# Optimization experiments

Measured on AMD Instinct MI355X. Metric: run time of the kernel, lower is better.

The kernel has to match this reference:

```python
import jax, jax.numpy as jnp
import numpy as np
import math

HEADS = 8
DIM_HEAD = 64

def setup_inputs() -> dict:
    key = jax.random.key(0)
    ks = jax.random.split(key, 6)
    B, L, D = 2, 2048, 512
    Ls = 1936
    inner = HEADS * DIM_HEAD  # 512
    x = jax.random.normal(ks[0], (B, L, D), dtype=jnp.float32)
    positions = jax.random.normal(ks[1], (B, Ls, 2), dtype=jnp.float32) * 10.0
    w_qkv = jax.random.normal(ks[2], (3 * inner, D), dtype=jnp.float32) * (1.0 / math.sqrt(D))
    w_out = jax.random.normal(ks[3], (D, inner), dtype=jnp.float32) * (1.0 / math.sqrt(inner))
    b_out = jnp.zeros((D,), dtype=jnp.float32)
    log_sigma = jnp.full((HEADS,), math.log(3.0), dtype=jnp.float32)
    global_bias = jnp.float32(0.0)
    return {"x": x, "positions": positions, "w_qkv": w_qkv, "w_out": w_out,
            "b_out": b_out, "log_sigma": log_sigma, "global_bias": global_bias,
            "num_spatial": Ls}

def reference(x, positions, w_qkv, w_out, b_out, log_sigma, global_bias, num_spatial):
    B, L, D = x.shape
    H, Dh = HEADS, DIM_HEAD
    scale = Dh ** (-0.5)
    # qkv projection: [B,L,3*H*Dh] -> q,k,v each [B,H,L,Dh]
    qkv = jnp.einsum('bld,ed->ble', x, w_qkv)
    q, k, v = jnp.split(qkv, 3, axis=-1)
    def heads(t):
        return t.reshape(B, L, H, Dh).transpose(0, 2, 1, 3)
    q, k, v = heads(q), heads(k), heads(v)
    attn = jnp.einsum('bhid,bhjd->bhij', q, k) * scale  # [B,H,L,L]
    # Gaussian distance bias on the spatial block, global_bias elsewhere
    Ls = num_spatial
    diff = positions[:, :, None, :] - positions[:, None, :, :]  # [B,Ls,Ls,2]
    dist_sq = jnp.sum(diff * diff, axis=-1)                     # [B,Ls,Ls]
    sigma_sq = jnp.exp(log_sigma) ** 2                          # [H]
    spatial_bias = -dist_sq[:, None] / (2.0 * sigma_sq[None, :, None, None])  # [B,H,Ls,Ls]
    full_bias = jnp.full((B, H, L, L), global_bias, dtype=x.dtype)
    full_bias = full_bias.at[:, :, :Ls, :Ls].set(spatial_bias)
    attn = jax.nn.softmax(attn + full_bias, axis=-1)
    out = jnp.einsum('bhij,bhjd->bhid', attn, v)  # [B,H,L,Dh]
    out = out.transpose(0, 2, 1, 3).reshape(B, L, H * Dh)
    return jnp.einsum('ble,de->bld', out, w_out) + b_out
```

## Files before the change

### kernel.cpp

```cpp
#include <hip/hip_runtime.h>
#include <stdint.h>
#include <stddef.h>

#define NB   2
#define NL   2048
#define ND   512
#define NH   8
#define DH   64
#define LOG2E 1.44269504f
#define NIT  16
#define RG_TOT 32768
#define JS   4

typedef __attribute__((ext_vector_type(8))) short bf16x8;
typedef __attribute__((ext_vector_type(4))) float f32x4;

__device__ __forceinline__ unsigned short f2bf(float f) {
  union { float f; unsigned int u; } c; c.f = f;
  unsigned int u = c.u;
  unsigned int r = u + 0x7fffu + ((u >> 16) & 1u);
  return (unsigned short)(r >> 16);
}

__device__ __forceinline__ float bf2f(unsigned short u) {
  union { unsigned int i; float f; } c; c.i = ((unsigned int)u) << 16; return c.f;
}

__device__ __forceinline__ float fexp2(float x) {
#if __has_builtin(__builtin_amdgcn_exp2f)
  return __builtin_amdgcn_exp2f(x);
#else
  return exp2f(x);
#endif
}

__device__ __forceinline__ void gl_lds16(const unsigned short* g, unsigned short* l) {
#if __has_builtin(__builtin_amdgcn_global_load_lds)
  __builtin_amdgcn_global_load_lds(
      (const __attribute__((address_space(1))) unsigned int*)g,
      (__attribute__((address_space(3))) unsigned int*)l, 16, 0, 0);
#else
  *(uint4*)l = *(const uint4*)g;
#endif
}

#define XC  524288
#define WQC 196608
#define WOC 65536
#define TOTC (XC + WQC + WOC)
__global__ void cvt_f32_bf16(const float* __restrict__ x, const float* __restrict__ wq,
                             const float* __restrict__ wo, const float* __restrict__ positions,
                             const int* __restrict__ ns_p,
                             unsigned short* __restrict__ xb, unsigned short* __restrict__ wqb,
                             unsigned short* __restrict__ wob, float* __restrict__ pospad) {
  int idx = blockIdx.x * 256 + threadIdx.x;
  if (idx < TOTC) {
    const float* src; unsigned short* dst; int off;
    if (idx < XC)            { src = x;  dst = xb;  off = idx; }
    else if (idx < XC + WQC) { src = wq; dst = wqb; off = idx - XC; }
    else                     { src = wo; dst = wob; off = idx - XC - WQC; }
    float4 f = ((const float4*)src)[off];
    ushort4 o;
    o.x = f2bf(f.x); o.y = f2bf(f.y); o.z = f2bf(f.z); o.w = f2bf(f.w);
    ((ushort4*)dst)[off] = o;
  } else {
    int i2 = idx - TOTC;
    if (i2 < NB * 1024) {
      int b = i2 >> 10;
      int jj = (i2 & 1023) * 2;
      int Ls = ns_p[0];
      float4 o = make_float4(0.f, 0.f, 0.f, 0.f);
      if (jj < Ls) { o.x = positions[((size_t)b * Ls + jj) * 2];
                     o.y = positions[((size_t)b * Ls + jj) * 2 + 1]; }
      if (jj + 1 < Ls) { o.z = positions[((size_t)b * Ls + jj + 1) * 2];
                         o.w = positions[((size_t)b * Ls + jj + 1) * 2 + 1]; }
      *(float4*)&pospad[((size_t)b * NL + jj) * 2] = o;
    }
  }
}

template<int MODE, int MT>
__global__ __launch_bounds__(256, 2) void gemm_bf16(
    const unsigned short* __restrict__ A, const unsigned short* __restrict__ Bm,
    const float* __restrict__ bias,
    unsigned short* __restrict__ qo, unsigned short* __restrict__ kp,
    unsigned short* __restrict__ vo, float* __restrict__ out, int K)
{
  constexpr int MB = MT / 32;
  constexpr int AC = MT * 4;
  constexpr int TC = AC + 512;
  __shared__ __align__(16) unsigned short S[MT * 32 + 128 * 32];
  const int tid = threadIdx.x, wid = tid >> 6, lane = tid & 63;
  const int quad = lane >> 4, l15 = lane & 15;
  const int m0 = blockIdx.x * MT, n0 = blockIdx.y * 128;
  const int wm = (wid >> 1) * (MT / 2), wn = (wid & 1) * 64;

  f32x4 acc[MB][4];
#pragma unroll
  for (int a = 0; a < MB; ++a)
#pragma unroll
    for (int b = 0; b < 4; ++b)
#pragma unroll
      for (int z = 0; z < 4; ++z) acc[a][b][z] = 0.f;

  for (int k0 = 0; k0 < K; k0 += 32) {
#pragma unroll
    for (int p = 0; p < TC / 256; ++p) {
      int c = p * 256 + wid * 64 + lane;
      if (c < AC) {
        int row = c >> 2, off = c & 3;
        gl_lds16(A + (size_t)(m0 + row) * K + k0 + off * 8, &S[c * 8]);
      } else {
        int cb = c - AC;
        int row = cb >> 2, off = cb & 3;
        gl_lds16(Bm + (size_t)(n0 + row) * K + k0 + off * 8, &S[c * 8]);
      }
    }
    __syncthreads();
    bf16x8 af[MB], bfr[4];
#pragma unroll
    for (int mb = 0; mb < MB; ++mb)
      af[mb] = *(const bf16x8*)&S[(wm + mb * 16 + l15) * 32 + quad * 8];
#pragma unroll
    for (int nb = 0; nb < 4; ++nb)
      bfr[nb] = *(const bf16x8*)&S[MT * 32 + (wn + nb * 16 + l15) * 32 + quad * 8];
#pragma unroll
    for (int mb = 0; mb < MB; ++mb)
#pragma unroll
      for (int nb = 0; nb < 4; ++nb)
        acc[mb][nb] = __builtin_amdgcn_mfma_f32_16x16x32_bf16(af[mb], bfr[nb], acc[mb][nb], 0, 0, 0);
    __syncthreads();
  }

  const float QSCALE = 0.125f * LOG2E;
#pragma unroll
  for (int mb = 0; mb < MB; ++mb) {
    int e0 = m0 + wm + mb * 16 + quad * 4;
    if (MODE == 0) {
      int s   = e0 >> 9;
      int hh  = (e0 >> 6) & 7;
      if (s == 1) {
        int kc  = mb >> 1;
        int q_t = ((mb & 1) << 1) + (quad >> 1);
        int par = quad & 1;
#pragma unroll
        for (int nb = 0; nb < 4; ++nb) {
          int token = n0 + wn + nb * 16 + l15;
          int bb = token >> 11, ll = token & 2047;
          int jt = ll >> 4;
          ushort4 o;
          o.x = f2bf(acc[mb][nb][0]);
          o.y = f2bf(acc[mb][nb][1]);
          o.z = f2bf(acc[mb][nb][2]);
          o.w = f2bf(acc[mb][nb][3]);
          size_t addr = (((size_t)(bb * NH + hh) * 128 + jt) * 2 + kc) * 512
                      + (q_t * 16 + l15) * 8 + par * 4;
          *(ushort4*)&kp[addr] = o;
        }
      } else {
        unsigned short* dst = (s == 0) ? qo : vo;
        float sc = (s == 0) ? QSCALE : 1.0f;
        int dh0 = e0 & 63;
#pragma unroll
        for (int nb = 0; nb < 4; ++nb) {
          int token = n0 + wn + nb * 16 + l15;
          int bb = token >> 11, ll = token & 2047;
          ushort4 o;
          o.x = f2bf(acc[mb][nb][0] * sc);
          o.y = f2bf(acc[mb][nb][1] * sc);
          o.z = f2bf(acc[mb][nb][2] * sc);
          o.w = f2bf(acc[mb][nb][3] * sc);
          *(ushort4*)&dst[(((size_t)bb * NH + hh) * NL + ll) * DH + dh0] = o;
        }
      }
    } else {
      float4 bv = *(const float4*)&bias[e0];
#pragma unroll
      for (int nb = 0; nb < 4; ++nb) {
        int token = n0 + wn + nb * 16 + l15;
        float4 o;
        o.x = acc[mb][nb][0] + bv.x;
        o.y = acc[mb][nb][1] + bv.y;
        o.z = acc[mb][nb][2] + bv.z;
        o.w = acc[mb][nb][3] + bv.w;
        *(float4*)&out[(size_t)token * ND + e0] = o;
      }
    }
  }
}

__global__ __launch_bounds__(256) void repack_v(const unsigned short* __restrict__ v,
                                                unsigned short* __restrict__ vp) {
  __shared__ unsigned short T[64][74];
  const int l0 = blockIdx.x * 64;
  const int bh = blockIdx.y;
  const unsigned short* src = v + ((size_t)bh * NL + l0) * DH;
  unsigned short* dst = vp + (size_t)bh * 131072 + (size_t)(l0 >> 5) * 2048;
#pragma unroll
  for (int p = 0; p < 2; ++p) {
    int c = p * 256 + threadIdx.x;
    int row = c >> 3, seg = c & 7;
    *(uint4*)&T[row][seg * 8] = *(const uint4*)(src + row * DH + seg * 8);
  }
  __syncthreads();
#pragma unroll
  for (int p = 0; p < 2; ++p) {
    int c = p * 256 + threadIdx.x;
    int l15 = c & 15, q = (c >> 4) & 3, dht = (c >> 6) & 3, jcl = c >> 8;
    unsigned short u[8];
#pragma unroll
    for (int t = 0; t < 8; ++t) u[t] = T[jcl * 32 + q * 8 + t][dht * 16 + l15];
    *(uint4*)(dst + (size_t)jcl * 2048 + dht * 512 + (q * 16 + l15) * 8) = *(uint4*)u;
  }
}

__global__ __launch_bounds__(256, 2) void flash_kernel(
    const unsigned short* __restrict__ qb, const unsigned short* __restrict__ kp,
    const unsigned short* __restrict__ vp, const float* __restrict__ pospad,
    const float* __restrict__ log_sigma, const float* __restrict__ gbias_p,
    const int* __restrict__ ns_p, unsigned short* __restrict__ Pb, float* __restrict__ rsbuf)
{
  const int it = blockIdx.x >> 2;
  const int js = blockIdx.x & 3;
  const int h  = blockIdx.y;
  const int b  = blockIdx.z;
  const int i0 = it * 128;
  const int jbase = js * (NL / JS);
  const int Ls = ns_p[0];
  const float gb  = gbias_p[0];
  const float sig = __expf(log_sigma[h]);
  const float CI  = LOG2E * 0.5f / (sig * sig);
  const float A2  = 2.0f * CI;
  const float LGB = LOG2E * gb;
  const float CBL = -8.0f * LOG2E + LGB;

  const int tid  = threadIdx.x;
  const int wid  = tid >> 6;
  const int lane = tid & 63;
  const int quad = lane >> 4;
  const int l15  = lane & 15;

  __shared__ __align__(16) unsigned short Ps[128][76];

  const size_t bh = (size_t)b * NH + h;
  const unsigned short* qbase = qb + (bh * NL + i0) * DH;
  const unsigned short* kpb   = kp + bh * 131072;
  const unsigned short* vpb   = vp + bh * 131072;
  const float* posb = pospad + (size_t)b * NL * 2;

  bf16x8 af[2][2];
#pragma unroll
  for (int mb = 0; mb < 2; ++mb)
#pragma unroll
    for (int kc = 0; kc < 2; ++kc)
      af[mb][kc] = *(const bf16x8*)(qbase + (size_t)(wid * 32 + mb * 16 + l15) * DH + kc * 32 + quad * 8);

  float pix_[2][4], piy_[2][4], riCm[2][4], ispf[2][4];
#pragma unroll
  for (int mb = 0; mb < 2; ++mb)
#pragma unroll
    for (int r = 0; r < 4; ++r) {
      int ig = i0 + wid * 32 + mb * 16 + quad * 4 + r;
      float2 p2 = *(const float2*)(posb + (size_t)ig * 2);
      pix_[mb][r] = p2.x; piy_[mb][r] = p2.y;
      ispf[mb][r] = (ig < Ls) ? 1.f : 0.f;
      riCm[mb][r] = -(CI * (p2.x * p2.x + p2.y * p2.y)) - LGB;
    }

  f32x4 accO[2][4];
  float rsum[2][4];
#pragma unroll
  for (int mb = 0; mb < 2; ++mb) {
#pragma unroll
    for (int d = 0; d < 4; ++d)
#pragma unroll
      for (int z = 0; z < 4; ++z) accO[mb][d][z] = 0.f;
#pragma unroll
    for (int r = 0; r < 4; ++r) rsum[mb][r] = 0.f;
  }

  for (int jt = 0; jt < NL / JS / 64; ++jt) {
    const int j0 = jbase + jt * 64;

    bf16x8 kf[4][2];
#pragma unroll
    for (int nb = 0; nb < 4; ++nb)
#pragma unroll
      for (int kc = 0; kc < 2; ++kc)
        kf[nb][kc] = *(const bf16x8*)(kpb + ((size_t)((j0 >> 4) + nb) * 2 + kc) * 512 + lane * 8);

    float pjx2[4], pjy2[4], rjC[4], jspf[4];
#pragma unroll
    for (int nb = 0; nb < 4; ++nb) {
      int jg = j0 + nb * 16 + l15;
      float2 p2 = *(const float2*)(posb + (size_t)jg * 2);
      pjx2[nb] = A2 * p2.x; pjy2[nb] = A2 * p2.y;
      rjC[nb]  = -(CI * (p2.x * p2.x + p2.y * p2.y));
      jspf[nb] = (jg < Ls) ? 1.f : 0.f;
    }

    f32x4 accS[2][4];
#pragma unroll
    for (int mb = 0; mb < 2; ++mb)
#pragma unroll
      for (int nb = 0; nb < 4; ++nb) {
#pragma unroll
        for (int z = 0; z < 4; ++z) accS[mb][nb][z] = 0.f;
        accS[mb][nb] = __builtin_amdgcn_mfma_f32_16x16x32_bf16(af[mb][0], kf[nb][0], accS[mb][nb], 0, 0, 0);
        accS[mb][nb] = __builtin_amdgcn_mfma_f32_16x16x32_bf16(af[mb][1], kf[nb][1], accS[mb][nb], 0, 0, 0);
      }

    bf16x8 vf[4][2];
#pragma unroll
    for (int dht = 0; dht < 4; ++dht)
#pragma unroll
      for (int jc = 0; jc < 2; ++jc)
        vf[dht][jc] = *(const bf16x8*)(vpb + ((size_t)((j0 >> 5) + jc) * 4 + dht) * 512 + lane * 8);

#pragma unroll
    for (int mb = 0; mb < 2; ++mb)
#pragma unroll
      for (int nb = 0; nb < 4; ++nb)
#pragma unroll
        for (int r = 0; r < 4; ++r) {
          float u = riCm[mb][r] + rjC[nb];
          u = __builtin_fmaf(piy_[mb][r], pjy2[nb], u);
          u = __builtin_fmaf(pix_[mb][r], pjx2[nb], u);
          float msp = ispf[mb][r] * jspf[nb];
          float t = __builtin_fmaf(msp, u, accS[mb][nb][r] + CBL);
          float p = fexp2(t);
          rsum[mb][r] += p;
          Ps[wid * 32 + mb * 16 + quad * 4 + r][nb * 16 + l15] = f2bf(p);
        }

    bf16x8 pf[2][2];
#pragma unroll
    for (int mb = 0; mb < 2; ++mb)
#pragma unroll
      for (int jc = 0; jc < 2; ++jc)
        pf[mb][jc] = *(const bf16x8*)&Ps[wid * 32 + mb * 16 + l15][jc * 32 + quad * 8];
#pragma unroll
    for (int mb = 0; mb < 2; ++mb)
#pragma unroll
      for (int dht = 0; dht < 4; ++dht) {
        accO[mb][dht] = __builtin_amdgcn_mfma_f32_16x16x32_bf16(pf[mb][0], vf[dht][0], accO[mb][dht], 0, 0, 0);
        accO[mb][dht] = __builtin_amdgcn_mfma_f32_16x16x32_bf16(pf[mb][1], vf[dht][1], accO[mb][dht], 0, 0, 0);
      }
  }

#pragma unroll
  for (int mb = 0; mb < 2; ++mb)
#pragma unroll
    for (int r = 0; r < 4; ++r) {
      float v = rsum[mb][r];
      v += __shfl_xor(v, 1);
      v += __shfl_xor(v, 2);
      v += __shfl_xor(v, 4);
      v += __shfl_xor(v, 8);
      rsum[mb][r] = v;
    }
  const size_t rgbase = (bh * NIT + it) * 128;
  const size_t poff = (size_t)js * RG_TOT * DH;
#pragma unroll
  for (int mb = 0; mb < 2; ++mb)
#pragma unroll
    for (int r = 0; r < 4; ++r) {
      int row = wid * 32 + mb * 16 + quad * 4 + r;
#pragma unroll
      for (int dht = 0; dht < 4; ++dht)
        Pb[poff + (rgbase + row) * DH + dht * 16 + l15] = f2bf(accO[mb][dht][r]);
      if (l15 == 0)
        rsbuf[(size_t)js * RG_TOT + rgbase + row] = rsum[mb][r];
    }
}

__global__ __launch_bounds__(256) void combine_kernel(const unsigned short* __restrict__ Pb,
                                                      const float* __restrict__ rsbuf,
                                                      unsigned short* __restrict__ attnb) {
  int idx = blockIdx.x * 256 + threadIdx.x;
  int rg = idx >> 4, c4 = idx & 15;
  float s0 = 0.f, s1 = 0.f, s2 = 0.f, s3 = 0.f, rsum = 0.f;
#pragma unroll
  for (int js = 0; js < JS; ++js) {
    ushort4 u = *(const ushort4*)&Pb[((size_t)js * RG_TOT + rg) * DH + c4 * 4];
    s0 += bf2f(u.x); s1 += bf2f(u.y); s2 += bf2f(u.z); s3 += bf2f(u.w);
    rsum += rsbuf[(size_t)js * RG_TOT + rg];
  }
  float rs = 1.0f / rsum;
  int bhm = rg >> 11;
  int l   = rg & 2047;
  int bb  = bhm >> 3, hh = bhm & 7;
  ushort4 o;
  o.x = f2bf(s0 * rs);
  o.y = f2bf(s1 * rs);
  o.z = f2bf(s2 * rs);
  o.w = f2bf(s3 * rs);
  *(ushort4*)&attnb[(((size_t)bb * NL + l) * ND) + hh * DH + c4 * 4] = o;
}

extern "C" void kernel_launch(void* const* d_in, const int* in_sizes, int n_in,
                              void* d_out, int out_size, void* d_ws, size_t ws_size,
                              hipStream_t stream) {
  const float* x         = (const float*)d_in[0];
  const float* positions = (const float*)d_in[1];
  const float* w_qkv     = (const float*)d_in[2];
  const float* w_out     = (const float*)d_in[3];
  const float* b_out     = (const float*)d_in[4];
  const float* log_sigma = (const float*)d_in[5];
  const float* gbias     = (const float*)d_in[6];
  const int*   ns        = (const int*)d_in[7];

  unsigned short* ws  = (unsigned short*)d_ws;
  unsigned short* xb  = ws;
  unsigned short* wob = xb  + 2097152;
  unsigned short* qbf = wob + 262144;
  unsigned short* kpf = qbf + 2097152;
  unsigned short* vbf = kpf + 2097152;
  unsigned short* vpf = vbf + 2097152;
  float* pospad = (float*)(vpf + 2097152);
  unsigned short* R   = (unsigned short*)(pospad + NB * NL * 2);
  unsigned short* wqb = R;
  unsigned short* Pb  = R;
  float* rsbuf = (float*)(Pb + (size_t)JS * RG_TOT * DH);

  cvt_f32_bf16<<<(TOTC + NB * 1024 + 255) / 256, 256, 0, stream>>>(
      x, w_qkv, w_out, positions, ns, xb, wqb, wob, pospad);

  dim3 g1((3 * NH * DH) / 128, NB * NL / 128);
  gemm_bf16<0, 128><<<g1, 256, 0, stream>>>(wqb, xb, nullptr, qbf, kpf, vbf, nullptr, ND);

  dim3 gr(NL / 64, NB * NH);
  repack_v<<<gr, 256, 0, stream>>>(vbf, vpf);

  dim3 g2((NL / 128) * JS, NH, NB);
  flash_kernel<<<g2, 256, 0, stream>>>(qbf, kpf, vpf, pospad, log_sigma, gbias, ns,
                                       Pb, rsbuf);

  combine_kernel<<<RG_TOT * 16 / 256, 256, 0, stream>>>(Pb, rsbuf, xb);

  dim3 g3(ND / 64, NB * NL / 128);
  gemm_bf16<1, 64><<<g3, 256, 0, stream>>>(wob, xb, b_out, nullptr, nullptr, nullptr,
                                           (float*)d_out, NH * DH);
}
```

Measured before the change: 154.2 us.

## Fold Gaussian distance bias into extra MFMA k-chunk and fuse combine into output GEMM

The spatial Gaussian bias is rewritten as a low-rank dot product: per-token extension vectors for queries and keys (split hi/lo bf16 for precision) are built in the repack kernel, so the flash kernel computes the bias with one extra MFMA per tile. This replaces the per-element FMA, position loads and masking in the softmax inner loop. The flash kernel is also transposed so S is computed as K·Q, which lets it use vectorized LDS writes and a cheaper row-sum reduction. The separate combine kernel is removed, and the cross-split reduction and normalization now happen inside the output GEMM's B-tile load. The cost is extra extension buffers, more work in the GEMM loader, and bf16 rounding error in the bias term, since large distance values pass through hi/lo bf16 splits.

```diff
diff --git a/kernel.cpp b/kernel.cpp
--- a/kernel.cpp
+++ b/kernel.cpp
@@ -8,7 +8,6 @@
 #define NH   8
 #define DH   64
 #define LOG2E 1.44269504f
-#define NIT  16
 #define RG_TOT 32768
 #define JS   4
 
@@ -24,6 +23,11 @@
 
 __device__ __forceinline__ float bf2f(unsigned short u) {
   union { unsigned int i; float f; } c; c.i = ((unsigned int)u) << 16; return c.f;
+}
+
+__device__ __forceinline__ void split2(float v, unsigned short& h, unsigned short& l) {
+  h = f2bf(v);
+  l = f2bf(v - bf2f(h));
 }
 
 __device__ __forceinline__ float fexp2(float x) {
@@ -79,53 +83,48 @@
   }
 }
 
-template<int MODE, int MT>
-__global__ __launch_bounds__(256, 2) void gemm_bf16(
+__global__ __launch_bounds__(256, 2) void gemm_qkv(
     const unsigned short* __restrict__ A, const unsigned short* __restrict__ Bm,
-    const float* __restrict__ bias,
     unsigned short* __restrict__ qo, unsigned short* __restrict__ kp,
-    unsigned short* __restrict__ vo, float* __restrict__ out, int K)
+    unsigned short* __restrict__ vo)
 {
-  constexpr int MB = MT / 32;
-  constexpr int AC = MT * 4;
-  constexpr int TC = AC + 512;
-  __shared__ __align__(16) unsigned short S[MT * 32 + 128 * 32];
+  __shared__ __align__(16) unsigned short S[128 * 32 + 128 * 32];
   const int tid = threadIdx.x, wid = tid >> 6, lane = tid & 63;
   const int quad = lane >> 4, l15 = lane & 15;
-  const int m0 = blockIdx.x * MT, n0 = blockIdx.y * 128;
-  const int wm = (wid >> 1) * (MT / 2), wn = (wid & 1) * 64;
-
-  f32x4 acc[MB][4];
-#pragma unroll
-  for (int a = 0; a < MB; ++a)
+  const int m0 = blockIdx.x * 128, n0 = blockIdx.y * 128;
+  const int wm = (wid >> 1) * 64, wn = (wid & 1) * 64;
+
+  f32x4 acc[4][4];
+#pragma unroll
+  for (int a = 0; a < 4; ++a)
 #pragma unroll
     for (int b = 0; b < 4; ++b)
 #pragma unroll
       for (int z = 0; z < 4; ++z) acc[a][b][z] = 0.f;
 
-  for (int k0 = 0; k0 < K; k0 += 32) {
-#pragma unroll
-    for (int p = 0; p < TC / 256; ++p) {
+  for (int k0 = 0; k0 < ND; k0 += 32) {
+#pragma unroll
+    for (int p = 0; p < 4; ++p) {
       int c = p * 256 + wid * 64 + lane;
-      if (c < AC) {
+      if (c < 512) {
         int row = c >> 2, off = c & 3;
-        gl_lds16(A + (size_t)(m0 + row) * K + k0 + off * 8, &S[c * 8]);
+        gl_lds16(A + (size_t)(m0 + row) * ND + k0 + off * 8, &S[c * 8]);
       } else {
-        int cb = c - AC;
+        int cb = c - 512;
         int row = cb >> 2, off = cb & 3;
-        gl_lds16(Bm + (size_t)(n0 + row) * K + k0 + off * 8, &S[c * 8]);
+        gl_lds16(Bm + (size_t)(n0 + row) * ND + k0 + off * 8, &S[c * 8]);
       }
     }
     __syncthreads();
-    bf16x8 af[MB], bfr[4];
-#pragma unroll
-    for (int mb = 0; mb < MB; ++mb)
+    bf16x8 af[4], bfr[4];
+#pragma unroll
+    for (int mb = 0; mb < 4; ++mb)
       af[mb] = *(const bf16x8*)&S[(wm + mb * 16 + l15) * 32 + quad * 8];
 #pragma unroll
     for (int nb = 0; nb < 4; ++nb)
-      bfr[nb] = *(const bf16x8*)&S[MT * 32 + (wn + nb * 16 + l15) * 32 + quad * 8];
-#pragma unroll
-    for (int mb = 0; mb < MB; ++mb)
+      bfr[nb] = *(const bf16x8*)&S[4096 + (wn + nb * 16 + l15) * 32 + quad * 8];
+#pragma unroll
+    for (int mb = 0; mb < 4; ++mb)
 #pragma unroll
       for (int nb = 0; nb < 4; ++nb)
         acc[mb][nb] = __builtin_amdgcn_mfma_f32_16x16x32_bf16(af[mb], bfr[nb], acc[mb][nb], 0, 0, 0);
@@ -134,91 +133,148 @@
 
   const float QSCALE = 0.125f * LOG2E;
 #pragma unroll
-  for (int mb = 0; mb < MB; ++mb) {
+  for (int mb = 0; mb < 4; ++mb) {
     int e0 = m0 + wm + mb * 16 + quad * 4;
-    if (MODE == 0) {
-      int s   = e0 >> 9;
-      int hh  = (e0 >> 6) & 7;
-      if (s == 1) {
-        int kc  = mb >> 1;
-        int q_t = ((mb & 1) << 1) + (quad >> 1);
-        int par = quad & 1;
-#pragma unroll
-        for (int nb = 0; nb < 4; ++nb) {
-          int token = n0 + wn + nb * 16 + l15;
-          int bb = token >> 11, ll = token & 2047;
-          int jt = ll >> 4;
-          ushort4 o;
-          o.x = f2bf(acc[mb][nb][0]);
-          o.y = f2bf(acc[mb][nb][1]);
-          o.z = f2bf(acc[mb][nb][2]);
-          o.w = f2bf(acc[mb][nb][3]);
-          size_t addr = (((size_t)(bb * NH + hh) * 128 + jt) * 2 + kc) * 512
-                      + (q_t * 16 + l15) * 8 + par * 4;
-          *(ushort4*)&kp[addr] = o;
-        }
-      } else {
-        unsigned short* dst = (s == 0) ? qo : vo;
-        float sc = (s == 0) ? QSCALE : 1.0f;
-        int dh0 = e0 & 63;
-#pragma unroll
-        for (int nb = 0; nb < 4; ++nb) {
-          int token = n0 + wn + nb * 16 + l15;
-          int bb = token >> 11, ll = token & 2047;
-          ushort4 o;
-          o.x = f2bf(acc[mb][nb][0] * sc);
-          o.y = f2bf(acc[mb][nb][1] * sc);
-          o.z = f2bf(acc[mb][nb][2] * sc);
-          o.w = f2bf(acc[mb][nb][3] * sc);
-          *(ushort4*)&dst[(((size_t)bb * NH + hh) * NL + ll) * DH + dh0] = o;
-        }
+    int s   = e0 >> 9;
+    int hh  = (e0 >> 6) & 7;
+    if (s == 1) {
+      int kc  = mb >> 1;
+      int q_t = ((mb & 1) << 1) + (quad >> 1);
+      int par = quad & 1;
+#pragma unroll
+      for (int nb = 0; nb < 4; ++nb) {
+        int token = n0 + wn + nb * 16 + l15;
+        int bb = token >> 11, ll = token & 2047;
+        int jt = ll >> 4;
+        ushort4 o;
+        o.x = f2bf(acc[mb][nb][0]);
+        o.y = f2bf(acc[mb][nb][1]);
+        o.z = f2bf(acc[mb][nb][2]);
+        o.w = f2bf(acc[mb][nb][3]);
+        size_t addr = (((size_t)(bb * NH + hh) * 128 + jt) * 2 + kc) * 512
+                    + (q_t * 16 + l15) * 8 + par * 4;
+        *(ushort4*)&kp[addr] = o;
       }
     } else {
-      float4 bv = *(const float4*)&bias[e0];
+      unsigned short* dst = (s == 0) ? qo : vo;
+      float sc = (s == 0) ? QSCALE : 1.0f;
+      int dh0 = e0 & 63;
 #pragma unroll
       for (int nb = 0; nb < 4; ++nb) {
         int token = n0 + wn + nb * 16 + l15;
-        float4 o;
-        o.x = acc[mb][nb][0] + bv.x;
-        o.y = acc[mb][nb][1] + bv.y;
-        o.z = acc[mb][nb][2] + bv.z;
-        o.w = acc[mb][nb][3] + bv.w;
-        *(float4*)&out[(size_t)token * ND + e0] = o;
+        int bb = token >> 11, ll = token & 2047;
+        ushort4 o;
+        o.x = f2bf(acc[mb][nb][0] * sc);
+        o.y = f2bf(acc[mb][nb][1] * sc);
+        o.z = f2bf(acc[mb][nb][2] * sc);
+        o.w = f2bf(acc[mb][nb][3] * sc);
+        *(ushort4*)&dst[(((size_t)bb * NH + hh) * NL + ll) * DH + dh0] = o;
       }
     }
   }
 }
 
-__global__ __launch_bounds__(256) void repack_v(const unsigned short* __restrict__ v,
-                                                unsigned short* __restrict__ vp) {
+__global__ __launch_bounds__(256) void repack_v(
+    const unsigned short* __restrict__ v, unsigned short* __restrict__ vp,
+    const float* __restrict__ pospad, const float* __restrict__ log_sigma,
+    const float* __restrict__ gbias_p, const int* __restrict__ ns_p,
+    unsigned short* __restrict__ kext, unsigned short* __restrict__ qext)
+{
   __shared__ unsigned short T[64][74];
   const int l0 = blockIdx.x * 64;
   const int bh = blockIdx.y;
+  const int b  = bh >> 3, h = bh & 7;
+  const int Ls = ns_p[0];
+  const float gb  = gbias_p[0];
+  const float sig = __expf(log_sigma[h]);
+  const float CI  = LOG2E * 0.5f / (sig * sig);
+  const float LGB = LOG2E * gb;
+  const float* posb = pospad + (size_t)b * NL * 2;
+  const int tid = threadIdx.x;
+
   const unsigned short* src = v + ((size_t)bh * NL + l0) * DH;
   unsigned short* dst = vp + (size_t)bh * 131072 + (size_t)(l0 >> 5) * 2048;
 #pragma unroll
   for (int p = 0; p < 2; ++p) {
-    int c = p * 256 + threadIdx.x;
+    int c = p * 256 + tid;
     int row = c >> 3, seg = c & 7;
     *(uint4*)&T[row][seg * 8] = *(const uint4*)(src + row * DH + seg * 8);
   }
   __syncthreads();
 #pragma unroll
   for (int p = 0; p < 2; ++p) {
-    int c = p * 256 + threadIdx.x;
+    int c = p * 256 + tid;
     int l15 = c & 15, q = (c >> 4) & 3, dht = (c >> 6) & 3, jcl = c >> 8;
     unsigned short u[8];
 #pragma unroll
     for (int t = 0; t < 8; ++t) u[t] = T[jcl * 32 + q * 8 + t][dht * 16 + l15];
     *(uint4*)(dst + (size_t)jcl * 2048 + dht * 512 + (q * 16 + l15) * 8) = *(uint4*)u;
   }
+
+  {
+    int jtl  = tid >> 6;
+    int lane = tid & 63;
+    int quad = lane >> 4, l15 = lane & 15;
+    int j = l0 + jtl * 16 + l15;
+    unsigned short bv[16];
+#pragma unroll
+    for (int z = 0; z < 16; ++z) bv[z] = 0;
+    if (j < Ls) {
+      float2 p2 = *(const float2*)(posb + (size_t)j * 2);
+      float rjC = -(CI * (p2.x * p2.x + p2.y * p2.y));
+      unsigned short one = f2bf(1.0f);
+      bv[0] = one; bv[1] = one;
+      split2(rjC, bv[2], bv[3]);
+      unsigned short Xh, Xl, Yh, Yl;
+      split2(2.0f * CI * p2.x, Xh, Xl);
+      split2(2.0f * CI * p2.y, Yh, Yl);
+      bv[4] = Xh; bv[5] = Xh; bv[6] = Xl;
+      bv[7] = Yh; bv[8] = Yh; bv[9] = Yl;
+    }
+    unsigned short o[8];
+#pragma unroll
+    for (int z = 0; z < 8; ++z) o[z] = bv[quad * 8 + z < 16 ? quad * 8 + z : 15];
+    if (quad >= 2) {
+#pragma unroll
+      for (int z = 0; z < 8; ++z) o[z] = 0;
+    }
+    *(uint4*)(kext + ((size_t)bh * 128 + (l0 >> 4) + jtl) * 512 + lane * 8) = *(uint4*)o;
+  }
+
+  {
+    int row = tid >> 2, seg = tid & 3;
+    int i = l0 + row;
+    unsigned short av[16];
+#pragma unroll
+    for (int z = 0; z < 16; ++z) av[z] = 0;
+    if (i < Ls) {
+      float2 p2 = *(const float2*)(posb + (size_t)i * 2);
+      float riCm = -(CI * (p2.x * p2.x + p2.y * p2.y)) - LGB;
+      unsigned short one = f2bf(1.0f);
+      split2(riCm, av[0], av[1]);
+      av[2] = one; av[3] = one;
+      unsigned short xh, xl, yh, yl;
+      split2(p2.x, xh, xl);
+      split2(p2.y, yh, yl);
+      av[4] = xh; av[5] = xl; av[6] = xh;
+      av[7] = yh; av[8] = yl; av[9] = yh;
+    }
+    unsigned short o[8];
+#pragma unroll
+    for (int z = 0; z < 8; ++z) o[z] = (seg * 8 + z < 16) ? av[seg * 8 + z] : 0;
+    if (seg >= 2) {
+#pragma unroll
+      for (int z = 0; z < 8; ++z) o[z] = 0;
+    }
+    *(uint4*)(qext + ((size_t)bh * NL + i) * 32 + seg * 8) = *(uint4*)o;
+  }
 }
 
 __global__ __launch_bounds__(256, 2) void flash_kernel(
-    const unsigned short* __restrict__ qb, const unsigned short* __restrict__ kp,
-    const unsigned short* __restrict__ vp, const float* __restrict__ pospad,
-    const float* __restrict__ log_sigma, const float* __restrict__ gbias_p,
-    const int* __restrict__ ns_p, unsigned short* __restrict__ Pb, float* __restrict__ rsbuf)
+    const unsigned short* __restrict__ qb, const unsigned short* __restrict__ qeb,
+    const unsigned short* __restrict__ kp, const unsigned short* __restrict__ keb,
+    const unsigned short* __restrict__ vp, const float* __restrict__ gbias_p,
+    unsigned short* __restrict__ Pb, float* __restrict__ rsbuf)
 {
   const int it = blockIdx.x >> 2;
   const int js = blockIdx.x & 3;
@@ -226,13 +282,7 @@
   const int b  = blockIdx.z;
   const int i0 = it * 128;
   const int jbase = js * (NL / JS);
-  const int Ls = ns_p[0];
-  const float gb  = gbias_p[0];
-  const float sig = __expf(log_sigma[h]);
-  const float CI  = LOG2E * 0.5f / (sig * sig);
-  const float A2  = 2.0f * CI;
-  const float LGB = LOG2E * gb;
-  const float CBL = -8.0f * LOG2E + LGB;
+  const float CBL = -8.0f * LOG2E + LOG2E * gbias_p[0];
 
   const int tid  = threadIdx.x;
   const int wid  = tid >> 6;
@@ -240,75 +290,37 @@
   const int quad = lane >> 4;
   const int l15  = lane & 15;
 
-  __shared__ __align__(16) unsigned short Ps[128][76];
+  __shared__ __align__(16) unsigned short Ps[128][78];
 
   const size_t bh = (size_t)b * NH + h;
-  const unsigned short* qbase = qb + (bh * NL + i0) * DH;
-  const unsigned short* kpb   = kp + bh * 131072;
-  const unsigned short* vpb   = vp + bh * 131072;
-  const float* posb = pospad + (size_t)b * NL * 2;
-
-  bf16x8 af[2][2];
-#pragma unroll
-  for (int mb = 0; mb < 2; ++mb)
+  const unsigned short* qbase  = qb  + (bh * NL + i0 + wid * 32) * DH;
+  const unsigned short* qebase = qeb + (bh * NL + i0 + wid * 32) * 32;
+  const unsigned short* kpb    = kp  + bh * 131072;
+  const unsigned short* kebb   = keb + bh * 65536;
+  const unsigned short* vpb    = vp  + bh * 131072;
+
+  bf16x8 qf[2][2], qfe[2];
+#pragma unroll
+  for (int ib = 0; ib < 2; ++ib) {
 #pragma unroll
     for (int kc = 0; kc < 2; ++kc)
-      af[mb][kc] = *(const bf16x8*)(qbase + (size_t)(wid * 32 + mb * 16 + l15) * DH + kc * 32 + quad * 8);
-
-  float pix_[2][4], piy_[2][4], riCm[2][4], ispf[2][4];
-#pragma unroll
-  for (int mb = 0; mb < 2; ++mb)
-#pragma unroll
-    for (int r = 0; r < 4; ++r) {
-      int ig = i0 + wid * 32 + mb * 16 + quad * 4 + r;
-      float2 p2 = *(const float2*)(posb + (size_t)ig * 2);
-      pix_[mb][r] = p2.x; piy_[mb][r] = p2.y;
-      ispf[mb][r] = (ig < Ls) ? 1.f : 0.f;
-      riCm[mb][r] = -(CI * (p2.x * p2.x + p2.y * p2.y)) - LGB;
-    }
-
-  f32x4 accO[2][4];
-  float rsum[2][4];
-#pragma unroll
-  for (int mb = 0; mb < 2; ++mb) {
-#pragma unroll
-    for (int d = 0; d < 4; ++d)
-#pragma unroll
-      for (int z = 0; z < 4; ++z) accO[mb][d][z] = 0.f;
-#pragma unroll
-    for (int r = 0; r < 4; ++r) rsum[mb][r] = 0.f;
-  }
+      qf[ib][kc] = *(const bf16x8*)(qbase + (size_t)(ib * 16 + l15) * DH + kc * 32 + quad * 8);
+    qfe[ib] = *(const bf16x8*)(qebase + (size_t)(ib * 16 + l15) * 32 + quad * 8);
+  }
+
+  f32x4 accO[4][2];
+  float rsum[2];
+#pragma unroll
+  for (int d = 0; d < 4; ++d)
+#pragma unroll
+    for (int ib = 0; ib < 2; ++ib)
+#pragma unroll
+      for (int z = 0; z < 4; ++z) accO[d][ib][z] = 0.f;
+  rsum[0] = 0.f; rsum[1] = 0.f;
 
   for (int jt = 0; jt < NL / JS / 64; ++jt) {
     const int j0 = jbase + jt * 64;
-
-    bf16x8 kf[4][2];
-#pragma unroll
-    for (int nb = 0; nb < 4; ++nb)
-#pragma unroll
-      for (int kc = 0; kc < 2; ++kc)
-        kf[nb][kc] = *(const bf16x8*)(kpb + ((size_t)((j0 >> 4) + nb) * 2 + kc) * 512 + lane * 8);
-
-    float pjx2[4], pjy2[4], rjC[4], jspf[4];
-#pragma unroll
-    for (int nb = 0; nb < 4; ++nb) {
-      int jg = j0 + nb * 16 + l15;
-      float2 p2 = *(const float2*)(posb + (size_t)jg * 2);
-      pjx2[nb] = A2 * p2.x; pjy2[nb] = A2 * p2.y;
-      rjC[nb]  = -(CI * (p2.x * p2.x + p2.y * p2.y));
-      jspf[nb] = (jg < Ls) ? 1.f : 0.f;
-    }
-
-    f32x4 accS[2][4];
-#pragma unroll
-    for (int mb = 0; mb < 2; ++mb)
-#pragma unroll
-      for (int nb = 0; nb < 4; ++nb) {
-#pragma unroll
-        for (int z = 0; z < 4; ++z) accS[mb][nb][z] = 0.f;
-        accS[mb][nb] = __builtin_amdgcn_mfma_f32_16x16x32_bf16(af[mb][0], kf[nb][0], accS[mb][nb], 0, 0, 0);
-        accS[mb][nb] = __builtin_amdgcn_mfma_f32_16x16x32_bf16(af[mb][1], kf[nb][1], accS[mb][nb], 0, 0, 0);
-      }
+    const int jt0 = j0 >> 4;
 
     bf16x8 vf[4][2];
 #pragma unroll
@@ -318,84 +330,150 @@
         vf[dht][jc] = *(const bf16x8*)(vpb + ((size_t)((j0 >> 5) + jc) * 4 + dht) * 512 + lane * 8);
 
 #pragma unroll
+    for (int jb = 0; jb < 4; ++jb) {
+      bf16x8 kf0 = *(const bf16x8*)(kpb + ((size_t)(jt0 + jb) * 2 + 0) * 512 + lane * 8);
+      bf16x8 kf1 = *(const bf16x8*)(kpb + ((size_t)(jt0 + jb) * 2 + 1) * 512 + lane * 8);
+      bf16x8 kfe = *(const bf16x8*)(kebb + (size_t)(jt0 + jb) * 512 + lane * 8);
+#pragma unroll
+      for (int ib = 0; ib < 2; ++ib) {
+        f32x4 accS;
+#pragma unroll
+        for (int z = 0; z < 4; ++z) accS[z] = 0.f;
+        accS = __builtin_amdgcn_mfma_f32_16x16x32_bf16(kf0, qf[ib][0], accS, 0, 0, 0);
+        accS = __builtin_amdgcn_mfma_f32_16x16x32_bf16(kf1, qf[ib][1], accS, 0, 0, 0);
+        accS = __builtin_amdgcn_mfma_f32_16x16x32_bf16(kfe, qfe[ib], accS, 0, 0, 0);
+        float p0 = fexp2(accS[0] + CBL);
+        float p1 = fexp2(accS[1] + CBL);
+        float p2 = fexp2(accS[2] + CBL);
+        float p3 = fexp2(accS[3] + CBL);
+        rsum[ib] += (p0 + p1) + (p2 + p3);
+        uint2 w;
+        w.x = (uint32_t)f2bf(p0) | ((uint32_t)f2bf(p1) << 16);
+        w.y = (uint32_t)f2bf(p2) | ((uint32_t)f2bf(p3) << 16);
+        *(uint2*)&Ps[wid * 32 + ib * 16 + l15][jb * 16 + quad * 4] = w;
+      }
+    }
+
+    bf16x8 pf[2][2];
+#pragma unroll
+    for (int ib = 0; ib < 2; ++ib)
+#pragma unroll
+      for (int jc = 0; jc < 2; ++jc)
+        pf[ib][jc] = *(const bf16x8*)&Ps[wid * 32 + ib * 16 + l15][jc * 32 + quad * 8];
+#pragma unroll
+    for (int dht = 0; dht < 4; ++dht)
+#pragma unroll
+      for (int ib = 0; ib < 2; ++ib) {
+        accO[dht][ib] = __builtin_amdgcn_mfma_f32_16x16x32_bf16(vf[dht][0], pf[ib][0], accO[dht][ib], 0, 0, 0);
+        accO[dht][ib] = __builtin_amdgcn_mfma_f32_16x16x32_bf16(vf[dht][1], pf[ib][1], accO[dht][ib], 0, 0, 0);
+      }
+  }
+
+  const size_t rgbase = bh * NL + i0;
+  const size_t poff = (size_t)js * RG_TOT * DH;
+#pragma unroll
+  for (int ib = 0; ib < 2; ++ib) {
+    float v = rsum[ib];
+    v += __shfl_xor(v, 16);
+    v += __shfl_xor(v, 32);
+    int irow = wid * 32 + ib * 16 + l15;
+    if (quad == 0)
+      rsbuf[(size_t)js * RG_TOT + rgbase + irow] = v;
+#pragma unroll
+    for (int dht = 0; dht < 4; ++dht) {
+      ushort4 o;
+      o.x = f2bf(accO[dht][ib][0]);
+      o.y = f2bf(accO[dht][ib][1]);
+      o.z = f2bf(accO[dht][ib][2]);
+      o.w = f2bf(accO[dht][ib][3]);
+      *(ushort4*)&Pb[poff + (rgbase + irow) * DH + dht * 16 + quad * 4] = o;
+    }
+  }
+}
+
+__global__ __launch_bounds__(256, 2) void gemm_out(
+    const unsigned short* __restrict__ A, const unsigned short* __restrict__ Pb,
+    const float* __restrict__ rsbuf, const float* __restrict__ bias,
+    float* __restrict__ out)
+{
+  __shared__ __align__(16) unsigned short S[64 * 32 + 128 * 32];
+  const int tid = threadIdx.x, wid = tid >> 6, lane = tid & 63;
+  const int quad = lane >> 4, l15 = lane & 15;
+  const int m0 = blockIdx.x * 64, n0 = blockIdx.y * 128;
+  const int wm = (wid >> 1) * 32, wn = (wid & 1) * 64;
+
+  f32x4 acc[2][4];
+#pragma unroll
+  for (int a = 0; a < 2; ++a)
+#pragma unroll
+    for (int b = 0; b < 4; ++b)
+#pragma unroll
+      for (int z = 0; z < 4; ++z) acc[a][b][z] = 0.f;
+
+  for (int k0 = 0; k0 < ND; k0 += 32) {
+    {
+      int c = wid * 64 + lane;
+      int row = c >> 2, off = c & 3;
+      gl_lds16(A + (size_t)(m0 + row) * ND + k0 + off * 8, &S[c * 8]);
+    }
+    int head = k0 >> 6;
+    int dhb  = k0 & 32;
+#pragma unroll
+    for (int p = 0; p < 2; ++p) {
+      int cb = p * 256 + tid;
+      int row = cb >> 2, off = cb & 3;
+      int token = n0 + row;
+      int bb = token >> 11, ll = token & 2047;
+      size_t rg = ((size_t)(bb * NH + head)) * NL + ll;
+      float rs = rsbuf[rg] + rsbuf[RG_TOT + rg] + rsbuf[2 * RG_TOT + rg] + rsbuf[3 * RG_TOT + rg];
+      float rinv = 1.0f / rs;
+      float s[8];
+#pragma unroll
+      for (int z = 0; z < 8; ++z) s[z] = 0.f;
+#pragma unroll
+      for (int jp = 0; jp < JS; ++jp) {
+        ushort4 u0 = *(const ushort4*)&Pb[((size_t)jp * RG_TOT + rg) * DH + dhb + off * 8];
+        ushort4 u1 = *(const ushort4*)&Pb[((size_t)jp * RG_TOT + rg) * DH + dhb + off * 8 + 4];
+        s[0] += bf2f(u0.x); s[1] += bf2f(u0.y); s[2] += bf2f(u0.z); s[3] += bf2f(u0.w);
+        s[4] += bf2f(u1.x); s[5] += bf2f(u1.y); s[6] += bf2f(u1.z); s[7] += bf2f(u1.w);
+      }
+      uint32_t w0 = (uint32_t)f2bf(s[0] * rinv) | ((uint32_t)f2bf(s[1] * rinv) << 16);
+      uint32_t w1 = (uint32_t)f2bf(s[2] * rinv) | ((uint32_t)f2bf(s[3] * rinv) << 16);
+      uint32_t w2 = (uint32_t)f2bf(s[4] * rinv) | ((uint32_t)f2bf(s[5] * rinv) << 16);
+      uint32_t w3 = (uint32_t)f2bf(s[6] * rinv) | ((uint32_t)f2bf(s[7] * rinv) << 16);
+      *(uint4*)&S[2048 + cb * 8] = make_uint4(w0, w1, w2, w3);
+    }
+    __syncthreads();
+    bf16x8 af[2], bfr[4];
+#pragma unroll
     for (int mb = 0; mb < 2; ++mb)
+      af[mb] = *(const bf16x8*)&S[(wm + mb * 16 + l15) * 32 + quad * 8];
+#pragma unroll
+    for (int nb = 0; nb < 4; ++nb)
+      bfr[nb] = *(const bf16x8*)&S[2048 + (wn + nb * 16 + l15) * 32 + quad * 8];
+#pragma unroll
+    for (int mb = 0; mb < 2; ++mb)
 #pragma unroll
       for (int nb = 0; nb < 4; ++nb)
-#pragma unroll
-        for (int r = 0; r < 4; ++r) {
-          float u = riCm[mb][r] + rjC[nb];
-          u = __builtin_fmaf(piy_[mb][r], pjy2[nb], u);
-          u = __builtin_fmaf(pix_[mb][r], pjx2[nb], u);
-          float msp = ispf[mb][r] * jspf[nb];
-          float t = __builtin_fmaf(msp, u, accS[mb][nb][r] + CBL);
-          float p = fexp2(t);
-          rsum[mb][r] += p;
-          Ps[wid * 32 + mb * 16 + quad * 4 + r][nb * 16 + l15] = f2bf(p);
-        }
-
-    bf16x8 pf[2][2];
-#pragma unroll
-    for (int mb = 0; mb < 2; ++mb)
-#pragma unroll
-      for (int jc = 0; jc < 2; ++jc)
-        pf[mb][jc] = *(const bf16x8*)&Ps[wid * 32 + mb * 16 + l15][jc * 32 + quad * 8];
-#pragma unroll
-    for (int mb = 0; mb < 2; ++mb)
-#pragma unroll
-      for (int dht = 0; dht < 4; ++dht) {
-        accO[mb][dht] = __builtin_amdgcn_mfma_f32_16x16x32_bf16(pf[mb][0], vf[dht][0], accO[mb][dht], 0, 0, 0);
-        accO[mb][dht] = __builtin_amdgcn_mfma_f32_16x16x32_bf16(pf[mb][1], vf[dht][1], accO[mb][dht], 0, 0, 0);
-      }
-  }
-
-#pragma unroll
-  for (int mb = 0; mb < 2; ++mb)
-#pragma unroll
-    for (int r = 0; r < 4; ++r) {
-      float v = rsum[mb][r];
-      v += __shfl_xor(v, 1);
-      v += __shfl_xor(v, 2);
-      v += __shfl_xor(v, 4);
-      v += __shfl_xor(v, 8);
-      rsum[mb][r] = v;
-    }
-  const size_t rgbase = (bh * NIT + it) * 128;
-  const size_t poff = (size_t)js * RG_TOT * DH;
-#pragma unroll
-  for (int mb = 0; mb < 2; ++mb)
-#pragma unroll
-    for (int r = 0; r < 4; ++r) {
-      int row = wid * 32 + mb * 16 + quad * 4 + r;
-#pragma unroll
-      for (int dht = 0; dht < 4; ++dht)
-        Pb[poff + (rgbase + row) * DH + dht * 16 + l15] = f2bf(accO[mb][dht][r]);
-      if (l15 == 0)
-        rsbuf[(size_t)js * RG_TOT + rgbase + row] = rsum[mb][r];
-    }
-}
-
-__global__ __launch_bounds__(256) void combine_kernel(const unsigned short* __restrict__ Pb,
-                                                      const float* __restrict__ rsbuf,
-                                                      unsigned short* __restrict__ attnb) {
-  int idx = blockIdx.x * 256 + threadIdx.x;
-  int rg = idx >> 4, c4 = idx & 15;
-  float s0 = 0.f, s1 = 0.f, s2 = 0.f, s3 = 0.f, rsum = 0.f;
-#pragma unroll
-  for (int js = 0; js < JS; ++js) {
-    ushort4 u = *(const ushort4*)&Pb[((size_t)js * RG_TOT + rg) * DH + c4 * 4];
-    s0 += bf2f(u.x); s1 += bf2f(u.y); s2 += bf2f(u.z); s3 += bf2f(u.w);
-    rsum += rsbuf[(size_t)js * RG_TOT + rg];
-  }
-  float rs = 1.0f / rsum;
-  int bhm = rg >> 11;
-  int l   = rg & 2047;
-  int bb  = bhm >> 3, hh = bhm & 7;
-  ushort4 o;
-  o.x = f2bf(s0 * rs);
-  o.y = f2bf(s1 * rs);
-  o.z = f2bf(s2 * rs);
-  o.w = f2bf(s3 * rs);
-  *(ushort4*)&attnb[(((size_t)bb * NL + l) * ND) + hh * DH + c4 * 4] = o;
+        acc[mb][nb] = __builtin_amdgcn_mfma_f32_16x16x32_bf16(af[mb], bfr[nb], acc[mb][nb], 0, 0, 0);
+    __syncthreads();
+  }
+
+#pragma unroll
+  for (int mb = 0; mb < 2; ++mb) {
+    int e0 = m0 + wm + mb * 16 + quad * 4;
+    float4 bv = *(const float4*)&bias[e0];
+#pragma unroll
+    for (int nb = 0; nb < 4; ++nb) {
+      int token = n0 + wn + nb * 16 + l15;
+      float4 o;
+      o.x = acc[mb][nb][0] + bv.x;
+      o.y = acc[mb][nb][1] + bv.y;
+      o.z = acc[mb][nb][2] + bv.z;
+      o.w = acc[mb][nb][3] + bv.w;
+      *(float4*)&out[(size_t)token * ND + e0] = o;
+    }
+  }
 }
 
 extern "C" void kernel_launch(void* const* d_in, const int* in_sizes, int n_in,
@@ -410,35 +488,33 @@
   const float* gbias     = (const float*)d_in[6];
   const int*   ns        = (const int*)d_in[7];
 
-  unsigned short* ws  = (unsigned short*)d_ws;
-  unsigned short* xb  = ws;
-  unsigned short* wob = xb  + 2097152;
-  unsigned short* qbf = wob + 262144;
-  unsigned short* kpf = qbf + 2097152;
-  unsigned short* vbf = kpf + 2097152;
-  unsigned short* vpf = vbf + 2097152;
-  float* pospad = (float*)(vpf + 2097152);
-  unsigned short* R   = (unsigned short*)(pospad + NB * NL * 2);
-  unsigned short* wqb = R;
-  unsigned short* Pb  = R;
+  unsigned short* ws   = (unsigned short*)d_ws;
+  unsigned short* xb   = ws;
+  unsigned short* wob  = xb   + 2097152;
+  unsigned short* qbf  = wob  + 262144;
+  unsigned short* kpf  = qbf  + 2097152;
+  unsigned short* vbf  = kpf  + 2097152;
+  unsigned short* vpf  = vbf  + 2097152;
+  unsigned short* qext = vpf  + 2097152;
+  unsigned short* kext = qext + 1048576;
+  float* pospad = (float*)(kext + 1048576);
+  unsigned short* R    = (unsigned short*)(pospad + NB * NL * 2);
+  unsigned short* wqb  = R;
+  unsigned short* Pb   = R;
   float* rsbuf = (float*)(Pb + (size_t)JS * RG_TOT * DH);
 
   cvt_f32_bf16<<<(TOTC + NB * 1024 + 255) / 256, 256, 0, stream>>>(
       x, w_qkv, w_out, positions, ns, xb, wqb, wob, pospad);
 
   dim3 g1((3 * NH * DH) / 128, NB * NL / 128);
-  gemm_bf16<0, 128><<<g1, 256, 0, stream>>>(wqb, xb, nullptr, qbf, kpf, vbf, nullptr, ND);
+  gemm_qkv<<<g1, 256, 0, stream>>>(wqb, xb, qbf, kpf, vbf);
 
   dim3 gr(NL / 64, NB * NH);
-  repack_v<<<gr, 256, 0, stream>>>(vbf, vpf);
+  repack_v<<<gr, 256, 0, stream>>>(vbf, vpf, pospad, log_sigma, gbias, ns, kext, qext);
 
   dim3 g2((NL / 128) * JS, NH, NB);
-  flash_kernel<<<g2, 256, 0, stream>>>(qbf, kpf, vpf, pospad, log_sigma, gbias, ns,
-                                       Pb, rsbuf);
-
-  combine_kernel<<<RG_TOT * 16 / 256, 256, 0, stream>>>(Pb, rsbuf, xb);
+  flash_kernel<<<g2, 256, 0, stream>>>(qbf, qext, kpf, kext, vpf, gbias, Pb, rsbuf);
 
   dim3 g3(ND / 64, NB * NL / 128);
-  gemm_bf16<1, 64><<<g3, 256, 0, stream>>>(wob, xb, b_out, nullptr, nullptr, nullptr,
-                                           (float*)d_out, NH * DH);
-}
+  gemm_out<<<g3, 256, 0, stream>>>(wob, Pb, rsbuf, b_out, (float*)d_out);
+}
```

New measurement: 167.0 us. 1.08x slower.
